# Kernel optimization log

Measured on AMD Instinct MI355X. Metric: run time of the kernel, lower is better.

The kernel has to match this reference:

```python
import jax, jax.numpy as jnp
import numpy as np

E = 2_000_000   # edges
N = 200_000     # nodes
E_DIM = 128     # edge feature dim
G_DIM = 256     # global/graph feature dim
B = 1024        # number of graphs (batch.max()+1)
EPS = 1e-6      # torch_scatter scatter_std eps


def setup_inputs() -> dict:
    key = jax.random.key(0)
    k1, k2, k3, k4 = jax.random.split(key, 4)
    e = jax.random.normal(k1, (E, E_DIM), dtype=jnp.float32)
    e_index = jax.random.randint(k2, (2, E), 0, N, dtype=jnp.int64)
    batch = jnp.sort(jax.random.randint(k3, (N,), 0, B, dtype=jnp.int64))
    fc_w = jax.random.normal(k4, (E_DIM * 4, G_DIM), dtype=jnp.float32) * 0.02
    fc_b = jnp.zeros((G_DIM,), dtype=jnp.float32)
    return {"e_index": e_index, "e": e, "batch": batch, "fc_w": fc_w, "fc_b": fc_b}


def reference(e_index, e, batch, fc_w, fc_b):
    # graph id per edge (via target node of each edge)
    e_batch = batch[e_index[1]]  # [E]

    count = jax.ops.segment_sum(jnp.ones((e.shape[0],), e.dtype), e_batch,
                                num_segments=B)[:, None]  # [B, 1]
    s = jax.ops.segment_sum(e, e_batch, num_segments=B)    # [B, D]

    # scatter(reduce='mean'): empty segments -> 0 (divide by clamped count)
    mean = s / jnp.maximum(count, 1.0)

    # scatter min/max: torch_scatter fills empty segments with 0
    mn = jax.ops.segment_min(e, e_batch, num_segments=B)
    mx = jax.ops.segment_max(e, e_batch, num_segments=B)
    empty = count == 0.0
    mn = jnp.where(empty, 0.0, mn)
    mx = jnp.where(empty, 0.0, mx)

    # scatter_std (unbiased, matches torch_scatter composite):
    # std = sqrt(sum((x - mean)^2) / (clamp(count-1, 1) + eps))
    diff = e - mean[e_batch]                               # [E, D]
    var_sum = jax.ops.segment_sum(diff * diff, e_batch, num_segments=B)
    denom = jnp.maximum(count - 1.0, 1.0) + EPS
    std = jnp.sqrt(var_sum / denom)

    g = jnp.concatenate([mean, mn, mx, std], axis=1)       # [B, 4D]
    return g @ fc_w + fc_b                                 # [B, G_DIM]
```

## Files before the change

### kernel.cpp

```cpp
#include <hip/hip_runtime.h>
#include <math.h>

#define DIMS 128
#define GD 256
#define MAXB 1024
#define NSLOT 8
#define PARTS 4
#define NBLK 256
#define SCH 8192

typedef float vfloat4 __attribute__((ext_vector_type(4)));

__device__ __forceinline__ float4 ldnt(const float* p) {
    vfloat4 v = __builtin_nontemporal_load(reinterpret_cast<const vfloat4*>(p));
    return make_float4(v.x, v.y, v.z, v.w);
}
__device__ __forceinline__ float4 f4_add(float4 a, float4 b) {
    return make_float4(a.x + b.x, a.y + b.y, a.z + b.z, a.w + b.w);
}
__device__ __forceinline__ float4 f4_min(float4 a, float4 b) {
    return make_float4(fminf(a.x, b.x), fminf(a.y, b.y), fminf(a.z, b.z), fminf(a.w, b.w));
}
__device__ __forceinline__ float4 f4_max(float4 a, float4 b) {
    return make_float4(fmaxf(a.x, b.x), fmaxf(a.y, b.y), fmaxf(a.z, b.z), fmaxf(a.w, b.w));
}

template <int OP>
__device__ __forceinline__ float4 comb(float4 a, float4 b) {
    if (OP == 0) return f4_add(a, b);
    if (OP == 1) return f4_min(a, b);
    return f4_max(a, b);
}

template <int OP>
__device__ __forceinline__ float4 slot_reduce(float4 v, float4* red) {
    int t = threadIdx.x;
    __syncthreads();
    red[t] = v;
    __syncthreads();
    for (int off = 128; off >= 32; off >>= 1) {
        if (t < off) red[t] = comb<OP>(red[t], red[t + off]);
        __syncthreads();
    }
    return red[t & 31];
}

#define ACC(v) do { \
    sm = f4_add(sm, v); \
    sq = f4_add(sq, make_float4((v).x*(v).x, (v).y*(v).y, (v).z*(v).z, (v).w*(v).w)); \
    mn = f4_min(mn, v); mx = f4_max(mx, v); } while (0)

__global__ void __launch_bounds__(256)
hist2_kernel(const int* __restrict__ e_index, const int* __restrict__ batch,
             int E, int* __restrict__ hist2, unsigned short* __restrict__ eb) {
    __shared__ int lh[MAXB];
    for (int i = threadIdx.x; i < MAXB; i += 256) lh[i] = 0;
    __syncthreads();
    int b = blockIdx.x;
    int CH = (E + NBLK - 1) / NBLK;
    int lo = b * CH;
    int hi = min(E, lo + CH);
    for (int j = lo + threadIdx.x; j < hi; j += 256) {
        int node = e_index[E + j];
        int g = batch[node];
        eb[j] = (unsigned short)g;
        atomicAdd(&lh[g], 1);
    }
    __syncthreads();
    for (int i = threadIdx.x; i < MAXB; i += 256)
        hist2[(size_t)b * MAXB + i] = lh[i];
}

__global__ void __launch_bounds__(1024)
scanall_kernel(int* __restrict__ hist2, int* __restrict__ count, int* __restrict__ offs) {
    int g = threadIdx.x;
    int s = 0;
#pragma unroll 1
    for (int b0 = 0; b0 < NBLK; b0 += 8) {
        int v[8];
#pragma unroll
        for (int i = 0; i < 8; ++i) v[i] = hist2[(size_t)(b0 + i) * MAXB + g];
#pragma unroll
        for (int i = 0; i < 8; ++i) { hist2[(size_t)(b0 + i) * MAXB + g] = s; s += v[i]; }
    }
    count[g] = s;
    __shared__ int tmp[MAXB];
    tmp[g] = s;
    __syncthreads();
    for (int d = 1; d < MAXB; d <<= 1) {
        int x = (g >= d) ? tmp[g - d] : 0;
        __syncthreads();
        tmp[g] += x;
        __syncthreads();
    }
    offs[g] = tmp[g] - s;
}

__global__ void __launch_bounds__(256)
scatter_kernel(const unsigned short* __restrict__ eb, const int* __restrict__ hist2,
               const int* __restrict__ offs, int E, int* __restrict__ perm) {
    __shared__ int lhist[MAXB];
    __shared__ int lofs[MAXB];
    __shared__ int lcur[MAXB];
    __shared__ int lbase[MAXB];
    __shared__ int ws[256];
    __shared__ int bin[SCH];
    int b = blockIdx.x;
    int t = threadIdx.x;
    int CH = (E + NBLK - 1) / NBLK;
    int lo = b * CH;
    int hi = min(E, lo + CH);

    for (int i = t; i < MAXB; i += 256) {
        lhist[i] = 0;
        lbase[i] = offs[i] + hist2[(size_t)b * MAXB + i];
    }
    __syncthreads();
    for (int j = lo + t; j < hi; j += 256) atomicAdd(&lhist[eb[j]], 1);
    __syncthreads();
    int base = t * 4;
    int c0 = lhist[base + 0], c1 = lhist[base + 1], c2 = lhist[base + 2], c3 = lhist[base + 3];
    int s0 = c0 + c1 + c2 + c3;
    ws[t] = s0;
    __syncthreads();
    for (int d = 1; d < 256; d <<= 1) {
        int x = (t >= d) ? ws[t - d] : 0;
        __syncthreads();
        ws[t] += x;
        __syncthreads();
    }
    int excl = ws[t] - s0;
    lofs[base + 0] = excl;
    lofs[base + 1] = excl + c0;
    lofs[base + 2] = excl + c0 + c1;
    lofs[base + 3] = excl + c0 + c1 + c2;
    lcur[base + 0] = excl;
    lcur[base + 1] = excl + c0;
    lcur[base + 2] = excl + c0 + c1;
    lcur[base + 3] = excl + c0 + c1 + c2;
    __syncthreads();
    for (int j = lo + t; j < hi; j += 256) {
        int g = eb[j];
        int r = atomicAdd(&lcur[g], 1);
        bin[r] = j;
    }
    __syncthreads();
    int grp = t >> 3, sub = t & 7;
    for (int g = grp; g < MAXB; g += 32) {
        int sfrom = lofs[g];
        int n = lcur[g] - sfrom;
        int dst = lbase[g];
        for (int k = sub; k < n; k += 8)
            perm[dst + k] = bin[sfrom + k];
    }
}

__global__ void __launch_bounds__(256)
reduce_kernel(const float* __restrict__ e, const int* __restrict__ perm,
              const int* __restrict__ offs, const int* __restrict__ count,
              float* __restrict__ pbuf) {
    int bid = blockIdx.x;
    int g = bid >> 2;
    int p = bid & 3;
    int start = offs[g];
    int cnt = count[g];
    int chunk = (cnt + PARTS - 1) / PARTS;
    int base = start + p * chunk;
    int cnt_p = cnt - p * chunk;
    if (cnt_p > chunk) cnt_p = chunk;
    if (cnt_p < 0) cnt_p = 0;
    const int* pp = perm + base;

    int c = threadIdx.x & 31;
    int s = threadIdx.x >> 5;

    float4 sm = make_float4(0.f, 0.f, 0.f, 0.f);
    float4 sq = make_float4(0.f, 0.f, 0.f, 0.f);
    float4 mn = make_float4(INFINITY, INFINITY, INFINITY, INFINITY);
    float4 mx = make_float4(-INFINITY, -INFINITY, -INFINITY, -INFINITY);

    int i = s;
    if (i + 3 * NSLOT < cnt_p) {
        int ia0 = pp[i], ia1 = pp[i + NSLOT], ia2 = pp[i + 2 * NSLOT], ia3 = pp[i + 3 * NSLOT];
        while (true) {
            int ni = i + 4 * NSLOT;
            int na0 = 0, na1 = 0, na2 = 0, na3 = 0;
            bool nok = (ni + 3 * NSLOT < cnt_p);
            if (nok) { na0 = pp[ni]; na1 = pp[ni + NSLOT]; na2 = pp[ni + 2 * NSLOT]; na3 = pp[ni + 3 * NSLOT]; }
            float4 v0 = ldnt(e + (size_t)ia0 * DIMS + c * 4);
            float4 v1 = ldnt(e + (size_t)ia1 * DIMS + c * 4);
            float4 v2 = ldnt(e + (size_t)ia2 * DIMS + c * 4);
            float4 v3 = ldnt(e + (size_t)ia3 * DIMS + c * 4);
            ACC(v0); ACC(v1); ACC(v2); ACC(v3);
            i = ni;
            if (!nok) break;
            ia0 = na0; ia1 = na1; ia2 = na2; ia3 = na3;
        }
    }
    for (; i < cnt_p; i += NSLOT) {
        int r = pp[i];
        float4 v = ldnt(e + (size_t)r * DIMS + c * 4);
        ACC(v);
    }

    __shared__ float4 red[256];
    float4 smr = slot_reduce<0>(sm, red);
    float4 mnr = slot_reduce<1>(mn, red);
    float4 mxr = slot_reduce<2>(mx, red);
    float4 sqr = slot_reduce<0>(sq, red);

    if (threadIdx.x < 32) {
        float* row = pbuf + (size_t)bid * (4 * DIMS);
        int d0 = c * 4;
        *reinterpret_cast<float4*>(row + 0 * DIMS + d0) = smr;
        *reinterpret_cast<float4*>(row + 1 * DIMS + d0) = mnr;
        *reinterpret_cast<float4*>(row + 2 * DIMS + d0) = mxr;
        *reinterpret_cast<float4*>(row + 3 * DIMS + d0) = sqr;
    }
}

__global__ void __launch_bounds__(256)
gemm_kernel(const float* __restrict__ pbuf, const int* __restrict__ count,
            const float* __restrict__ w, const float* __restrict__ bias,
            float* __restrict__ out, int B) {
    __shared__ float gl[8 * 512];
    int r0 = blockIdx.x * 8;
    int t = threadIdx.x;
#pragma unroll
    for (int q = 0; q < 4; ++q) {
        int pair = q * 256 + t;
        int r = pair >> 7;
        int d = pair & 127;
        int g = r0 + r;
        float sm = 0.f, sq = 0.f, mnv = INFINITY, mxv = -INFINITY;
        int cnt = 0;
        if (g < B) {
            cnt = count[g];
            const float* pb = pbuf + (size_t)g * PARTS * 512;
#pragma unroll
            for (int p = 0; p < PARTS; ++p) {
                const float* row = pb + p * 512;
                sm += row[d];
                mnv = fminf(mnv, row[128 + d]);
                mxv = fmaxf(mxv, row[256 + d]);
                sq += row[384 + d];
            }
        }
        float fc = (float)cnt;
        float fcm = fmaxf(fc, 1.0f);
        float mean = sm / fcm;
        float vs = fmaxf(sq - sm * mean, 0.f);
        float sd = sqrtf(vs / (fmaxf(fc - 1.0f, 1.0f) + 1e-6f));
        if (cnt == 0) { mnv = 0.f; mxv = 0.f; }
        gl[r * 512 + 0 * 128 + d] = mean;
        gl[r * 512 + 1 * 128 + d] = mnv;
        gl[r * 512 + 2 * 128 + d] = mxv;
        gl[r * 512 + 3 * 128 + d] = sd;
    }
    __syncthreads();

    int col = t;
    float acc[8];
    float bv = bias[col];
#pragma unroll
    for (int r = 0; r < 8; ++r) acc[r] = bv;
#pragma unroll 4
    for (int k = 0; k < 512; ++k) {
        float wv = w[k * GD + col];
#pragma unroll
        for (int r = 0; r < 8; ++r) acc[r] += gl[r * 512 + k] * wv;
    }
#pragma unroll
    for (int r = 0; r < 8; ++r) {
        int rr = r0 + r;
        if (rr < B) out[(size_t)rr * GD + col] = acc[r];
    }
}

extern "C" void kernel_launch(void* const* d_in, const int* in_sizes, int n_in,
                              void* d_out, int out_size, void* d_ws, size_t ws_size,
                              hipStream_t stream) {
    const int*   e_index = (const int*)d_in[0];
    const float* e       = (const float*)d_in[1];
    const int*   batch   = (const int*)d_in[2];
    const float* fc_w    = (const float*)d_in[3];
    const float* fc_b    = (const float*)d_in[4];
    float* out = (float*)d_out;

    int E = in_sizes[1] / DIMS;
    int B = out_size / GD;

    int* hist2 = (int*)d_ws;
    int* count = hist2 + (size_t)NBLK * MAXB;
    int* offs  = count + MAXB;
    unsigned short* eb = (unsigned short*)(offs + MAXB);
    int* perm  = (int*)(eb + (((size_t)E + 1) & ~(size_t)1));
    float* pbuf = (float*)(perm + E);

    hist2_kernel<<<NBLK, 256, 0, stream>>>(e_index, batch, E, hist2, eb);
    scanall_kernel<<<1, MAXB, 0, stream>>>(hist2, count, offs);
    scatter_kernel<<<NBLK, 256, 0, stream>>>(eb, hist2, offs, E, perm);
    reduce_kernel<<<B * PARTS, 256, 0, stream>>>(e, perm, offs, count, pbuf);
    gemm_kernel<<<(B + 7) / 8, 256, 0, stream>>>(pbuf, count, fc_w, fc_b, out, B);
}
```

Baseline: 285.7 us.

## Parallelize histogram scan across blocks and fold global offset scan into scatter

Replaces the single-block scan over all per-block histograms with a 1024-block column scan, one block per graph id, that writes exclusive per-block prefixes and per-graph counts. Each scatter block now recomputes the global exclusive offsets from the counts with its own shared-memory scan, and block 0 writes offs for the reduce kernel. The aim is to remove the serial single-block kernel that walked 256 rows, at the cost of redundant offset scans in every scatter block and strided column loads in the new scan kernel.

Measured after the change: 267.0 us. 6.5% less time.

```diff
diff --git a/kernel.cpp b/kernel.cpp
--- a/kernel.cpp
+++ b/kernel.cpp
@@ -71,34 +71,28 @@
         hist2[(size_t)b * MAXB + i] = lh[i];
 }
 
-__global__ void __launch_bounds__(1024)
-scanall_kernel(int* __restrict__ hist2, int* __restrict__ count, int* __restrict__ offs) {
-    int g = threadIdx.x;
-    int s = 0;
-#pragma unroll 1
-    for (int b0 = 0; b0 < NBLK; b0 += 8) {
-        int v[8];
-#pragma unroll
-        for (int i = 0; i < 8; ++i) v[i] = hist2[(size_t)(b0 + i) * MAXB + g];
-#pragma unroll
-        for (int i = 0; i < 8; ++i) { hist2[(size_t)(b0 + i) * MAXB + g] = s; s += v[i]; }
-    }
-    count[g] = s;
-    __shared__ int tmp[MAXB];
-    tmp[g] = s;
-    __syncthreads();
-    for (int d = 1; d < MAXB; d <<= 1) {
-        int x = (g >= d) ? tmp[g - d] : 0;
-        __syncthreads();
-        tmp[g] += x;
-        __syncthreads();
-    }
-    offs[g] = tmp[g] - s;
+__global__ void __launch_bounds__(256)
+colscan_kernel(int* __restrict__ hist2, int* __restrict__ count) {
+    int g = blockIdx.x;
+    int t = threadIdx.x;
+    int v = hist2[(size_t)t * MAXB + g];
+    __shared__ int ws[256];
+    ws[t] = v;
+    __syncthreads();
+    for (int d = 1; d < 256; d <<= 1) {
+        int x = (t >= d) ? ws[t - d] : 0;
+        __syncthreads();
+        ws[t] += x;
+        __syncthreads();
+    }
+    hist2[(size_t)t * MAXB + g] = ws[t] - v;
+    if (t == 255) count[g] = ws[255];
 }
 
 __global__ void __launch_bounds__(256)
 scatter_kernel(const unsigned short* __restrict__ eb, const int* __restrict__ hist2,
-               const int* __restrict__ offs, int E, int* __restrict__ perm) {
+               const int* __restrict__ count, int E,
+               int* __restrict__ perm, int* __restrict__ offs) {
     __shared__ int lhist[MAXB];
     __shared__ int lofs[MAXB];
     __shared__ int lcur[MAXB];
@@ -110,15 +104,34 @@
     int CH = (E + NBLK - 1) / NBLK;
     int lo = b * CH;
     int hi = min(E, lo + CH);
-
-    for (int i = t; i < MAXB; i += 256) {
-        lhist[i] = 0;
-        lbase[i] = offs[i] + hist2[(size_t)b * MAXB + i];
-    }
-    __syncthreads();
+    int base = t * 4;
+
+    int g0 = count[base + 0], g1 = count[base + 1], g2 = count[base + 2], g3 = count[base + 3];
+    int gsum = g0 + g1 + g2 + g3;
+    ws[t] = gsum;
+    __syncthreads();
+    for (int d = 1; d < 256; d <<= 1) {
+        int x = (t >= d) ? ws[t - d] : 0;
+        __syncthreads();
+        ws[t] += x;
+        __syncthreads();
+    }
+    int gexcl = ws[t] - gsum;
+    int ob0 = gexcl, ob1 = gexcl + g0, ob2 = gexcl + g0 + g1, ob3 = gexcl + g0 + g1 + g2;
+    if (b == 0) {
+        offs[base + 0] = ob0; offs[base + 1] = ob1;
+        offs[base + 2] = ob2; offs[base + 3] = ob3;
+    }
+    lbase[base + 0] = ob0 + hist2[(size_t)b * MAXB + base + 0];
+    lbase[base + 1] = ob1 + hist2[(size_t)b * MAXB + base + 1];
+    lbase[base + 2] = ob2 + hist2[(size_t)b * MAXB + base + 2];
+    lbase[base + 3] = ob3 + hist2[(size_t)b * MAXB + base + 3];
+    lhist[base + 0] = 0; lhist[base + 1] = 0; lhist[base + 2] = 0; lhist[base + 3] = 0;
+    __syncthreads();
+
     for (int j = lo + t; j < hi; j += 256) atomicAdd(&lhist[eb[j]], 1);
     __syncthreads();
-    int base = t * 4;
+
     int c0 = lhist[base + 0], c1 = lhist[base + 1], c2 = lhist[base + 2], c3 = lhist[base + 3];
     int s0 = c0 + c1 + c2 + c3;
     ws[t] = s0;
@@ -139,12 +152,14 @@
     lcur[base + 2] = excl + c0 + c1;
     lcur[base + 3] = excl + c0 + c1 + c2;
     __syncthreads();
+
     for (int j = lo + t; j < hi; j += 256) {
         int g = eb[j];
         int r = atomicAdd(&lcur[g], 1);
         bin[r] = j;
     }
     __syncthreads();
+
     int grp = t >> 3, sub = t & 7;
     for (int g = grp; g < MAXB; g += 32) {
         int sfrom = lofs[g];
@@ -298,8 +313,8 @@
     float* pbuf = (float*)(perm + E);
 
     hist2_kernel<<<NBLK, 256, 0, stream>>>(e_index, batch, E, hist2, eb);
-    scanall_kernel<<<1, MAXB, 0, stream>>>(hist2, count, offs);
-    scatter_kernel<<<NBLK, 256, 0, stream>>>(eb, hist2, offs, E, perm);
+    colscan_kernel<<<MAXB, 256, 0, stream>>>(hist2, count);
+    scatter_kernel<<<NBLK, 256, 0, stream>>>(eb, hist2, count, E, perm, offs);
     reduce_kernel<<<B * PARTS, 256, 0, stream>>>(e, perm, offs, count, pbuf);
     gemm_kernel<<<(B + 7) / 8, 256, 0, stream>>>(pbuf, count, fc_w, fc_b, out, B);
 }
```
